# Kernel tuning notes

Measured on AMD Instinct MI355X. Metric: run time of the kernel, lower is better.

Reference implementation:

```python
import jax, jax.numpy as jnp
import numpy as np

BS, T, G, C = 64, 128, 36, 256
H = 256          # gaze LSTM hidden
P = 256          # spatial projected size
PT = 256         # temporal projected size
Q = 16           # queue size
NC = 10          # num classes
NEG = -1e9


def setup_inputs() -> dict:
    key = jax.random.key(0)
    ks = jax.random.split(key, 40)
    s = 0.02
    D = C + H
    inp = {
        'cnn_feat_seq': jax.random.normal(ks[0], (BS, T, G, C), jnp.float32),
        'gaze_seq': jax.random.normal(ks[1], (BS, T, 3), jnp.float32),
        # init-hidden / init-cell MLPs (Linear(3,H), Tanh, Linear(H,H), Tanh)
        'init_h_w1': jax.random.normal(ks[2], (H, 3)) * s, 'init_h_b1': jnp.zeros((H,)),
        'init_h_w2': jax.random.normal(ks[3], (H, H)) * s, 'init_h_b2': jnp.zeros((H,)),
        'init_c_w1': jax.random.normal(ks[4], (H, 3)) * s, 'init_c_b1': jnp.zeros((H,)),
        'init_c_w2': jax.random.normal(ks[5], (H, H)) * s, 'init_c_b2': jnp.zeros((H,)),
        # LSTM (input 3, hidden H), torch gate order i,f,g,o
        'lstm_wih': jax.random.normal(ks[6], (4 * H, 3)) * s, 'lstm_whh': jax.random.normal(ks[7], (4 * H, H)) * s,
        'lstm_bih': jnp.zeros((4 * H,)), 'lstm_bhh': jnp.zeros((4 * H,)),
        # spatial attention
        'sa_wl': jax.random.normal(ks[8], (P, H)) * s, 'sa_bl': jnp.zeros((P,)),
        'sa_wc': jax.random.normal(ks[9], (P, C)) * s, 'sa_bc': jnp.zeros((P,)),
        'sa_wz': jax.random.normal(ks[10], (P,)) * s,
        # temporal attention
        'ta_wl': jax.random.normal(ks[11], (PT, H)) * s, 'ta_bl': jnp.zeros((PT,)),
        'ta_wv': jax.random.normal(ks[12], (PT, C)) * s, 'ta_bv': jnp.zeros((PT,)),
        'ta_wz': jax.random.normal(ks[13], (PT,)) * s,
        # MLP classifier: Linear(D,D) -> Linear(D,D) -> Linear(D,NC), no nonlinearity
        'mlp_w1': jax.random.normal(ks[14], (D, D)) * s, 'mlp_b1': jnp.zeros((D,)),
        'mlp_w2': jax.random.normal(ks[15], (D, D)) * s, 'mlp_b2': jnp.zeros((D,)),
        'mlp_w3': jax.random.normal(ks[16], (NC, D)) * s, 'mlp_b3': jnp.zeros((NC,)),
    }
    return inp


def _forward(cnn_feat_seq, gaze_seq,
             init_h_w1, init_h_b1, init_h_w2, init_h_b2,
             init_c_w1, init_c_b1, init_c_w2, init_c_b2,
             lstm_wih, lstm_whh, lstm_bih, lstm_bhh,
             sa_wl, sa_bl, sa_wc, sa_bc, sa_wz,
             ta_wl, ta_bl, ta_wv, ta_bv, ta_wz,
             mlp_w1, mlp_b1, mlp_w2, mlp_b2, mlp_w3, mlp_b3):
    bs, num_frame = gaze_seq.shape[0], gaze_seq.shape[1]
    mean_gaze = jnp.mean(gaze_seq, axis=1)  # (bs, 3)
    # init MLP ends with Tanh, and forward applies F.tanh again
    h0 = jnp.tanh(jnp.tanh(jnp.tanh(mean_gaze @ init_h_w1.T + init_h_b1) @ init_h_w2.T + init_h_b2))
    c0 = jnp.tanh(jnp.tanh(jnp.tanh(mean_gaze @ init_c_w1.T + init_c_b1) @ init_c_w2.T + init_c_b2))
    buf_s0 = jnp.zeros((Q, bs, C), cnn_feat_seq.dtype)
    buf_h0 = jnp.zeros((Q, bs, H), cnn_feat_seq.dtype)
    qidx = jnp.arange(Q)

    def step(carry, xs):
        h, c, buf_s, buf_h, i = carry
        feat, gaze = xs  # (bs,G,C), (bs,3)
        # --- spatial additive attention over grids ---
        Hp = h @ sa_wl.T + sa_bl                                  # (bs,P)
        Vp = jnp.einsum('bgc,pc->bgp', feat, sa_wc) + sa_bc       # (bs,G,P)
        zs = jnp.tanh(Hp[:, None, :] + Vp) @ sa_wz                # (bs,G)
        sw = jax.nn.softmax(zs, axis=1)
        spat = jnp.einsum('bgc,bg->bc', feat, sw)                 # (bs,C)
        # --- rolling queues (newest last) ---
        buf_s = jnp.concatenate([buf_s[1:], spat[None]], axis=0)
        buf_h = jnp.concatenate([buf_h[1:], h[None]], axis=0)
        count = jnp.minimum(i + 1, Q)
        mask = qidx >= (Q - count)                                # (Q,) valid slots
        # --- temporal additive attention over queue ---
        Hq = jnp.einsum('qbh,ph->qbp', buf_h, ta_wl) + ta_bl
        Vq = jnp.einsum('qbc,pc->qbp', buf_s, ta_wv) + ta_bv
        zt = jnp.tanh(Hq + Vq) @ ta_wz                            # (Q,bs)
        zt = jnp.where(mask[:, None], zt, NEG)
        tw = jax.nn.softmax(zt, axis=0)
        temp = jnp.einsum('qbc,qb->bc', buf_s, tw)                # (bs,C)
        # --- one LSTM step on gaze ---
        gates = gaze @ lstm_wih.T + lstm_bih + h @ lstm_whh.T + lstm_bhh
        gi, gf, gg, go = jnp.split(gates, 4, axis=-1)
        c = jax.nn.sigmoid(gf) * c + jax.nn.sigmoid(gi) * jnp.tanh(gg)
        h = jax.nn.sigmoid(go) * jnp.tanh(c)
        # --- classifier on concat(temporal_feat, lstm_hidden) ---
        fc = jnp.concatenate([temp, h], axis=1)                   # (bs, C+H)
        pred = ((fc @ mlp_w1.T + mlp_b1) @ mlp_w2.T + mlp_b2) @ mlp_w3.T + mlp_b3
        return (h, c, buf_s, buf_h, i + 1), pred

    feats_t = jnp.swapaxes(cnn_feat_seq, 0, 1)  # (T,bs,G,C)
    gaze_t = jnp.swapaxes(gaze_seq, 0, 1)       # (T,bs,3)
    _, preds = jax.lax.scan(step, (h0, c0, buf_s0, buf_h0, jnp.int32(0)), (feats_t, gaze_t))
    # torch cats (1,bs,NC) pieces along dim=1 -> (1, T*bs, NC)
    return preds.reshape(1, num_frame * bs, NC)


def reference(cnn_feat_seq, gaze_seq,
              init_h_w1, init_h_b1, init_h_w2, init_h_b2,
              init_c_w1, init_c_b1, init_c_w2, init_c_b2,
              lstm_wih, lstm_whh, lstm_bih, lstm_bhh,
              sa_wl, sa_bl, sa_wc, sa_bc, sa_wz,
              ta_wl, ta_bl, ta_wv, ta_bv, ta_wz,
              mlp_w1, mlp_b1, mlp_w2, mlp_b2, mlp_w3, mlp_b3):
    return _forward(cnn_feat_seq, gaze_seq,
                    init_h_w1, init_h_b1, init_h_w2, init_h_b2,
                    init_c_w1, init_c_b1, init_c_w2, init_c_b2,
                    lstm_wih, lstm_whh, lstm_bih, lstm_bhh,
                    sa_wl, sa_bl, sa_wc, sa_bc, sa_wz,
                    ta_wl, ta_bl, ta_wv, ta_bv, ta_wz,
                    mlp_w1, mlp_b1, mlp_w2, mlp_b2, mlp_w3, mlp_b3)
```

## Files before the change

kernel.cpp:

```cpp
#include <hip/hip_runtime.h>
#include <cstdint>
#include <cstddef>

#define BSZ 64
#define TT  128
#define GG  36
#define CC  256
#define HH  256
#define QQ  16
#define NCLS 10
#define NROW 8192

using short8  = __attribute__((ext_vector_type(8))) short;
using f32x4   = __attribute__((ext_vector_type(4))) float;
using half2_t = __attribute__((ext_vector_type(2))) _Float16;
typedef unsigned int u32;
typedef unsigned short u16;

#define OFF_WI    0u
#define OFF_WF    131072u
#define OFF_WG    262144u
#define OFF_WO    393216u
#define OFF_SAWL  524288u
#define OFF_TAWL  655360u
#define OFF_TAWV  786432u
#define OFF_SAWC  917504u
#define OFF_W32   1048576u
#define OFF_WC    1069056u
#define OFF_BC    1089536u
#define OFF_H0F16 1089792u
#define OFF_C0    1122560u
#define OFF_HSEQ  1188096u
#define OFF_HSEQB 9642240u
#define OFF_HPSA  13869312u
#define OFF_HQ    22257920u
#define OFF_SPAT  30646528u
#define OFF_SPATB 39035136u
#define OFF_ZSC   43229440u
#define WS_NEEDED 43262208u

__device__ __forceinline__ float rcp_fast(float x){
#if __has_builtin(__builtin_amdgcn_rcpf)
  return __builtin_amdgcn_rcpf(x);
#else
  return 1.f/x;
#endif
}
__device__ __forceinline__ float fast_sig(float x){ return rcp_fast(1.f+__expf(-x)); }
__device__ __forceinline__ float fast_tanh(float x){ float e=__expf(2.f*x); return 1.f-2.f*rcp_fast(e+1.f); }
__device__ __forceinline__ u16 f2bf(float f){
  u32 u = __builtin_bit_cast(u32, f);
  u += 0x7fffu + ((u>>16)&1u);
  return (u16)(u>>16);
}
__device__ __forceinline__ float bf2f(u16 b){
  u32 u = ((u32)b)<<16; return __builtin_bit_cast(float, u);
}
__device__ __forceinline__ u32 cvtpk_bf16(float a, float b){
  u32 p;
  asm("v_cvt_pk_bf16_f32 %0, %1, %2" : "=v"(p) : "v"(a), "v"(b));
  return p;
}
__device__ __forceinline__ u32 packf16(float a, float b){
  half2_t h; h.x = (_Float16)a; h.y = (_Float16)b;
  return __builtin_bit_cast(u32, h);
}
__device__ __forceinline__ float dot2(u32 w, u32 h, float acc){
#if __has_builtin(__builtin_amdgcn_fdot2)
  return __builtin_amdgcn_fdot2(__builtin_bit_cast(half2_t, w),
                                __builtin_bit_cast(half2_t, h), acc, false);
#else
  half2_t a = __builtin_bit_cast(half2_t, w), b = __builtin_bit_cast(half2_t, h);
  return acc + (float)a.x*(float)b.x + (float)a.y*(float)b.y;
#endif
}
__device__ __forceinline__ f32x4 mfma16(short8 a, short8 b, f32x4 c){
  return __builtin_amdgcn_mfma_f32_16x16x32_bf16(a, b, c, 0, 0, 0);
}

__global__ void __launch_bounds__(256) k_prep1(const float* __restrict__ whh,
    const float* __restrict__ sawl, const float* __restrict__ tawl,
    const float* __restrict__ tawv, const float* __restrict__ sawc,
    const float* __restrict__ w3, const float* __restrict__ w2, char* ws){
  int blk = blockIdx.x, tid = threadIdx.x;
  if (blk < 512){
    u32* wq = (u32*)ws;
    for (int rr = 0; rr < 2; ++rr){
      int row = blk*2 + rr;
      float v  = whh[row*256 + tid];
      float vn = __shfl_down(v, 1);
      if ((tid & 1) == 0){
        int typ = row >> 8;
        int j   = row & 255;
        wq[typ*32768 + (tid>>1)*256 + j] = packf16(v, vn);
      }
    }
  } else if (blk < 544){
    int rel = blk - 512;
    int mat = rel >> 3;
    const float* src; u16* dst;
    if (mat==0){ src=sawl; dst=(u16*)(ws+OFF_SAWL); }
    else if (mat==1){ src=tawl; dst=(u16*)(ws+OFF_TAWL); }
    else if (mat==2){ src=tawv; dst=(u16*)(ws+OFF_TAWV); }
    else { src=sawc; dst=(u16*)(ws+OFF_SAWC); }
    int base = (rel & 7)*8192 + tid;
    for (int i = 0; i < 32; ++i){ int e = base + i*256; dst[e] = f2bf(src[e]); }
  } else {
    int idx = (blk-544)*256 + tid;
    int o = idx >> 9, k2 = idx & 511;
    float acc = 0.f;
    for (int m = 0; m < 512; ++m) acc = fmaf(w3[o*512+m], w2[m*512+k2], acc);
    ((float*)(ws+OFF_W32))[idx] = acc;
  }
}

__global__ void __launch_bounds__(256) k_prep2(const float* __restrict__ w1,
    const float* __restrict__ b1, const float* __restrict__ w3,
    const float* __restrict__ b2, const float* __restrict__ b3,
    const float* __restrict__ gaze,
    const float* __restrict__ ihw1, const float* __restrict__ ihb1,
    const float* __restrict__ ihw2, const float* __restrict__ ihb2,
    const float* __restrict__ icw1, const float* __restrict__ icb1,
    const float* __restrict__ icw2, const float* __restrict__ icb2,
    char* ws){
  int blk = blockIdx.x, tid = threadIdx.x;
  const float* W32 = (const float*)(ws+OFF_W32);
  if (blk < 20){
    int idx = blk*256 + tid; int o = idx>>9, k = idx&511;
    float acc = 0.f;
    for (int m = 0; m < 512; ++m) acc = fmaf(W32[o*512+m], w1[m*512+k], acc);
    ((float*)(ws+OFF_WC))[idx] = acc;
  } else if (blk == 20){
    if (tid < 10){
      float acc = b3[tid];
      for (int m = 0; m < 512; ++m) acc = fmaf(W32[tid*512+m], b1[m], acc);
      for (int m = 0; m < 512; ++m) acc = fmaf(w3[tid*512+m], b2[m], acc);
      ((float*)(ws+OFF_BC))[tid] = acc;
    }
  } else {
    int b = blk - 21;
    __shared__ float red0[128], red1[128], red2[128];
    __shared__ float mg[3];
    __shared__ float x1[256];
    if (tid < 128){
      const float* gp = gaze + b*384 + tid*3;
      red0[tid] = gp[0]; red1[tid] = gp[1]; red2[tid] = gp[2];
    }
    __syncthreads();
    for (int s = 64; s >= 1; s >>= 1){
      if (tid < s){ red0[tid]+=red0[tid+s]; red1[tid]+=red1[tid+s]; red2[tid]+=red2[tid+s]; }
      __syncthreads();
    }
    if (tid == 0){ mg[0]=red0[0]*(1.f/128.f); mg[1]=red1[0]*(1.f/128.f); mg[2]=red2[0]*(1.f/128.f); }
    __syncthreads();
    for (int which = 0; which < 2; ++which){
      const float* aw1 = which? icw1 : ihw1; const float* ab1 = which? icb1 : ihb1;
      const float* aw2 = which? icw2 : ihw2; const float* ab2 = which? icb2 : ihb2;
      float v = fast_tanh(fmaf(aw1[tid*3+2],mg[2], fmaf(aw1[tid*3+1],mg[1], fmaf(aw1[tid*3],mg[0], ab1[tid]))));
      x1[tid] = v;
      __syncthreads();
      float acc = ab2[tid];
      for (int k = 0; k < 256; ++k) acc = fmaf(aw2[tid*256+k], x1[k], acc);
      float h0 = fast_tanh(fast_tanh(acc));
      if (which == 0){
        float* hseq = (float*)(ws+OFF_HSEQ);
        hseq[(size_t)(0*64 + b)*256 + tid] = h0;
        float hn = __shfl_down(h0, 1);
        if ((tid&1)==0){
          ((u32*)(ws+OFF_HSEQB))[((size_t)(0*64+b)*256 + tid)>>1] = ((u32)f2bf(hn)<<16) | f2bf(h0);
          ((u32*)(ws+OFF_H0F16))[b*128 + (tid>>1)] = packf16(h0, hn);
        }
      } else {
        ((float*)(ws+OFF_C0))[b*256 + tid] = h0;
      }
      __syncthreads();
    }
  }
}

__global__ void __launch_bounds__(512, 2) k_lstm(const float* __restrict__ gaze,
    const float* __restrict__ wih, const float* __restrict__ bih,
    const float* __restrict__ bhh, char* ws){
  int b = blockIdx.x, tid = threadIdx.x;
  int half = tid >> 8;
  int j = tid & 255;
  __shared__ u32 lds_w[16*2048];
  __shared__ __align__(16) u32 hbuf[2][128];
  __shared__ float p_lds[256];
  __shared__ float g_lds[384];

  const u32* wq = (const u32*)ws;
  const u32* wA = wq + (half ? 1 : 0) * 32768;
  const u32* wB = wq + (half ? 3 : 2) * 32768;
  u32 w0[128], w1r[64];
#pragma unroll
  for (int c = 0; c < 128; ++c) w0[c] = wA[c*256 + j];
#pragma unroll
  for (int c = 0; c < 64; ++c)  w1r[c] = wB[c*256 + j];
#pragma unroll
  for (int cq = 0; cq < 16; ++cq)
#pragma unroll
    for (int q = 0; q < 4; ++q)
      lds_w[cq*2048 + tid*4 + q] = wB[(64 + cq*4 + q)*256 + j];

  if (tid < 384) g_lds[tid] = gaze[b*384 + tid];
  if (tid < 128) hbuf[0][tid] = ((const u32*)(ws+OFF_H0F16))[b*128 + tid];
  float creg = half ? ((const float*)(ws+OFF_C0))[b*256 + j] : 0.f;

  int rA = half ? 256 + j : j;
  int rB = half ? 768 + j : 512 + j;
  float baseA = bih[rA] + bhh[rA];
  float baseB = bih[rB] + bhh[rB];
  float uA0 = wih[rA*3], uA1 = wih[rA*3+1], uA2 = wih[rA*3+2];
  float uB0 = wih[rB*3], uB1 = wih[rB*3+1], uB2 = wih[rB*3+2];

  float* hseq = (float*)(ws+OFF_HSEQ);
  u32* hseqb = (u32*)(ws+OFF_HSEQB);
  __syncthreads();

  for (int t = 0; t < 128; ++t){
    int cur = t & 1, nxt = cur ^ 1;
    float g0 = g_lds[t*3], g1 = g_lds[t*3+1], g2 = g_lds[t*3+2];
    float aA0 = fmaf(uA2,g2, fmaf(uA1,g1, fmaf(uA0,g0, baseA))), aA1 = 0.f;
    float aB0 = fmaf(uB2,g2, fmaf(uB1,g1, fmaf(uB0,g0, baseB))), aB1 = 0.f;
#pragma unroll
    for (int c4 = 0; c4 < 32; ++c4){
      uint4 h4 = *reinterpret_cast<const uint4*>(&hbuf[cur][c4*4]);
      u32 wb0, wb1, wb2, wb3;
      if (c4 < 16){
        wb0 = w1r[c4*4]; wb1 = w1r[c4*4+1]; wb2 = w1r[c4*4+2]; wb3 = w1r[c4*4+3];
      } else {
        uint4 wv = *reinterpret_cast<const uint4*>(&lds_w[(c4-16)*2048 + tid*4]);
        wb0 = wv.x; wb1 = wv.y; wb2 = wv.z; wb3 = wv.w;
      }
      aA0 = dot2(w0[c4*4+0], h4.x, aA0); aB0 = dot2(wb0, h4.x, aB0);
      aA1 = dot2(w0[c4*4+1], h4.y, aA1); aB1 = dot2(wb1, h4.y, aB1);
      aA0 = dot2(w0[c4*4+2], h4.z, aA0); aB0 = dot2(wb2, h4.z, aB0);
      aA1 = dot2(w0[c4*4+3], h4.w, aA1); aB1 = dot2(wb3, h4.w, aB1);
    }
    float aA = aA0 + aA1, aB = aB0 + aB1;
    if (half == 0){
      p_lds[j] = fast_sig(aA) * fast_tanh(aB);
    }
    __syncthreads();
    if (half == 1){
      float p = p_lds[j];
      creg = fmaf(fast_sig(aA), creg, p);
      float hv = fast_sig(aB) * fast_tanh(creg);
      float hn = __shfl_down(hv, 1);
      if ((j & 1) == 0){
        hbuf[nxt][j>>1] = packf16(hv, hn);
        hseqb[(((size_t)(t+1)*64 + b)*256 + j)>>1] = ((u32)f2bf(hn)<<16) | f2bf(hv);
      }
      hseq[((size_t)(t+1)*64 + b)*256 + j] = hv;
    }
    __syncthreads();
  }
}

__global__ void __launch_bounds__(256) k_proj1(const float* __restrict__ sabl,
    const float* __restrict__ sabc, const float* __restrict__ tabl,
    const float* __restrict__ tabv, char* ws){
  int bx = blockIdx.x, which = blockIdx.y;
  const u16* A = (const u16*)(ws+OFF_HSEQB);
  const u16* B = (const u16*)(ws + (which? OFF_TAWL : OFF_SAWL));
  float* Out   = (float*)(ws + (which? OFF_HQ : OFF_HPSA));
  const float* bp1 = which? tabl : sabl;
  const float* bp2 = which? tabv : sabc;
  int tid = threadIdx.x, w = tid>>6, l = tid&63;
  int lr = l&15, lk = l>>4;
  int rb = bx*64;
  short8 afr[4][8];
#pragma unroll
  for (int m = 0; m < 4; ++m)
#pragma unroll
    for (int k = 0; k < 8; ++k)
      afr[m][k] = *(const short8*)(const void*)(A + (size_t)(rb + m*16 + lr)*256 + k*32 + lk*8);
#pragma unroll
  for (int n = 0; n < 4; ++n){
    int cb = w*64 + n*16;
    int col = cb + lr;
    float bias = bp1[col] + bp2[col];
    f32x4 a0 = {0.f,0.f,0.f,0.f}, a1 = a0, a2 = a0, a3 = a0;
#pragma unroll
    for (int k = 0; k < 8; ++k){
      short8 bf = *(const short8*)(const void*)(B + (size_t)col*256 + k*32 + lk*8);
      a0 = mfma16(afr[0][k], bf, a0);
      a1 = mfma16(afr[1][k], bf, a1);
      a2 = mfma16(afr[2][k], bf, a2);
      a3 = mfma16(afr[3][k], bf, a3);
    }
#pragma unroll
    for (int q = 0; q < 4; ++q){
      Out[(size_t)(rb + 0*16 + lk*4 + q)*256 + col] = a0[q] + bias;
      Out[(size_t)(rb + 1*16 + lk*4 + q)*256 + col] = a1[q] + bias;
      Out[(size_t)(rb + 2*16 + lk*4 + q)*256 + col] = a2[q] + bias;
      Out[(size_t)(rb + 3*16 + lk*4 + q)*256 + col] = a3[q] + bias;
    }
  }
}

__global__ void __launch_bounds__(256) k_spatial(const float* __restrict__ feat,
    const float* __restrict__ sawz, char* ws){
  int blk = blockIdx.x;
  int tid = threadIdx.x, w = tid>>6, l = tid&63;
  int lr = l&15, lk = l>>4;
  __shared__ __align__(16) u16 featb[84*264];
  __shared__ float hp[2][256];
  __shared__ float wzs[256];
  __shared__ float zsbuf[2][4][48];
  __shared__ float swl[2][36];
  const float* hpsa = (const float*)(ws+OFF_HPSA);
#pragma unroll
  for (int rr = 0; rr < 2; ++rr){
    int r = blk*2 + rr;
    int t = r >> 6, b = r & 63;
    const float* fb = feat + ((size_t)(b*128 + t))*9216;
#pragma unroll
    for (int i = 0; i < 9; ++i){
      int e = tid + i*256;
      int g = e >> 6, cp4 = e & 63;
      float4 v = *(const float4*)(fb + g*256 + cp4*4);
      uint2 pp;
      pp.x = cvtpk_bf16(v.x, v.y);
      pp.y = cvtpk_bf16(v.z, v.w);
      *reinterpret_cast<uint2*>(&featb[(rr*36 + g)*264 + cp4*4]) = pp;
    }
    hp[rr][tid] = hpsa[(size_t)r*256 + tid];
  }
  wzs[tid] = sawz[tid];
  __syncthreads();
  const u16* Bw = (const u16*)(ws+OFF_SAWC);
#pragma unroll
  for (int rr = 0; rr < 2; ++rr){
    short8 afr[3][8];
#pragma unroll
    for (int m = 0; m < 3; ++m)
#pragma unroll
      for (int k = 0; k < 8; ++k)
        afr[m][k] = *(const short8*)(const void*)(featb + (rr*36 + m*16 + lr)*264 + k*32 + lk*8);
    float zacc[3][4] = {{0.f}};
#pragma unroll
    for (int n = 0; n < 4; ++n){
      int col = w*64 + n*16 + lr;
      float hpl = hp[rr][col], wzv = wzs[col];
      f32x4 a0 = {0.f,0.f,0.f,0.f}, a1 = a0, a2 = a0;
#pragma unroll
      for (int k = 0; k < 8; ++k){
        short8 bf = *(const short8*)(const void*)(Bw + (size_t)col*256 + k*32 + lk*8);
        a0 = mfma16(afr[0][k], bf, a0);
        a1 = mfma16(afr[1][k], bf, a1);
        a2 = mfma16(afr[2][k], bf, a2);
      }
#pragma unroll
      for (int q = 0; q < 4; ++q){
        zacc[0][q] += fast_tanh(a0[q] + hpl)*wzv;
        zacc[1][q] += fast_tanh(a1[q] + hpl)*wzv;
        zacc[2][q] += fast_tanh(a2[q] + hpl)*wzv;
      }
    }
#pragma unroll
    for (int m = 0; m < 3; ++m)
#pragma unroll
      for (int q = 0; q < 4; ++q){
        float v = zacc[m][q];
        v += __shfl_xor(v, 1); v += __shfl_xor(v, 2);
        v += __shfl_xor(v, 4); v += __shfl_xor(v, 8);
        if (lr == 0) zsbuf[rr][w][m*16 + lk*4 + q] = v;
      }
  }
  __syncthreads();
  {
    int rr = w & 1;
    float z = (l < 36)? zsbuf[rr][0][l]+zsbuf[rr][1][l]+zsbuf[rr][2][l]+zsbuf[rr][3][l] : -1e30f;
    float mx = z;
    for (int d = 1; d < 64; d <<= 1) mx = fmaxf(mx, __shfl_xor(mx, d));
    float e = (l < 36)? __expf(z - mx) : 0.f;
    float s = e;
    for (int d = 1; d < 64; d <<= 1) s += __shfl_xor(s, d);
    if (w < 2 && l < 36) swl[rr][l] = e * rcp_fast(s);
  }
  __syncthreads();
#pragma unroll
  for (int rr = 0; rr < 2; ++rr){
    int r = blk*2 + rr;
    float acc = 0.f;
#pragma unroll
    for (int g = 0; g < 36; ++g)
      acc = fmaf(swl[rr][g], bf2f(featb[(rr*36 + g)*264 + tid]), acc);
    ((float*)(ws+OFF_SPAT))[(size_t)r*256 + tid] = acc;
    float an = __shfl_down(acc, 1);
    if ((tid&1)==0)
      ((u32*)(ws+OFF_SPATB))[((size_t)r*256 + tid)>>1] = cvtpk_bf16(acc, an);
  }
}

__global__ void __launch_bounds__(256) k_proj2(const float* __restrict__ tawz, char* ws){
  int bx = blockIdx.x;
  int tid = threadIdx.x, w = tid>>6, l = tid&63;
  int lr = l&15, lk = l>>4;
  int rb = bx*64;
  const u16* A = (const u16*)(ws+OFF_SPATB);
  const u16* B = (const u16*)(ws+OFF_TAWV);
  const float* Hq = (const float*)(ws+OFF_HQ);
  __shared__ float zbuf[4][64];
  short8 afr[4][8];
#pragma unroll
  for (int m = 0; m < 4; ++m)
#pragma unroll
    for (int k = 0; k < 8; ++k)
      afr[m][k] = *(const short8*)(const void*)(A + (size_t)(rb + m*16 + lr)*256 + k*32 + lk*8);
  float racc[4][4] = {{0.f}};
#pragma unroll
  for (int n = 0; n < 4; ++n){
    int col = w*64 + n*16 + lr;
    float tzl = tawz[col];
    f32x4 a0 = {0.f,0.f,0.f,0.f}, a1 = a0, a2 = a0, a3 = a0;
#pragma unroll
    for (int k = 0; k < 8; ++k){
      short8 bf = *(const short8*)(const void*)(B + (size_t)col*256 + k*32 + lk*8);
      a0 = mfma16(afr[0][k], bf, a0);
      a1 = mfma16(afr[1][k], bf, a1);
      a2 = mfma16(afr[2][k], bf, a2);
      a3 = mfma16(afr[3][k], bf, a3);
    }
#pragma unroll
    for (int q = 0; q < 4; ++q){
      racc[0][q] += fast_tanh(a0[q] + Hq[(size_t)(rb + 0*16 + lk*4 + q)*256 + col]) * tzl;
      racc[1][q] += fast_tanh(a1[q] + Hq[(size_t)(rb + 1*16 + lk*4 + q)*256 + col]) * tzl;
      racc[2][q] += fast_tanh(a2[q] + Hq[(size_t)(rb + 2*16 + lk*4 + q)*256 + col]) * tzl;
      racc[3][q] += fast_tanh(a3[q] + Hq[(size_t)(rb + 3*16 + lk*4 + q)*256 + col]) * tzl;
    }
  }
#pragma unroll
  for (int m = 0; m < 4; ++m)
#pragma unroll
    for (int q = 0; q < 4; ++q){
      float v = racc[m][q];
      v += __shfl_xor(v, 1); v += __shfl_xor(v, 2);
      v += __shfl_xor(v, 4); v += __shfl_xor(v, 8);
      if (lr == 0) zbuf[w][m*16 + lk*4 + q] = v;
    }
  __syncthreads();
  if (tid < 64)
    ((float*)(ws+OFF_ZSC))[rb + tid] = zbuf[0][tid]+zbuf[1][tid]+zbuf[2][tid]+zbuf[3][tid];
}

__global__ void __launch_bounds__(256) k_final(float* __restrict__ out, char* ws){
  int bx = blockIdx.x;
  int b = bx & 63, tb = bx >> 6;
  int t0 = tb*8;
  int tid = threadIdx.x;
  int wv = tid>>6, l = tid&63;
  __shared__ float spw[23][256];
  __shared__ float zw[23];
  __shared__ float WcL[5120];
  __shared__ float bcL[10];
  __shared__ float w16[16];
  __shared__ float wpart[4][10];
  const float* spat = (const float*)(ws+OFF_SPAT);
  const float* zsc  = (const float*)(ws+OFF_ZSC);
  const float* hseq = (const float*)(ws+OFF_HSEQ);
  const float* Wc   = (const float*)(ws+OFF_WC);
#pragma unroll
  for (int i = 0; i < 20; ++i) WcL[tid + i*256] = Wc[tid + i*256];
  if (tid < 10) bcL[tid] = ((const float*)(ws+OFF_BC))[tid];
  for (int i = 0; i < 23; ++i){
    int tau = t0 - 15 + i;
    spw[i][tid] = (tau >= 0)? spat[(size_t)(tau*64 + b)*256 + tid] : 0.f;
  }
  if (tid < 23){
    int tau = t0 - 15 + tid;
    zw[tid] = (tau >= 0)? zsc[tau*64 + b] : -1e9f;
  }
  __syncthreads();
  for (int dt = 0; dt < 8; ++dt){
    int t = t0 + dt;
    if (wv == 0 && l < 16){
      float z = zw[dt + l];
      float mx = z;
      mx = fmaxf(mx, __shfl_xor(mx,1)); mx = fmaxf(mx, __shfl_xor(mx,2));
      mx = fmaxf(mx, __shfl_xor(mx,4)); mx = fmaxf(mx, __shfl_xor(mx,8));
      float e = __expf(z - mx);
      float s = e;
      s += __shfl_xor(s,1); s += __shfl_xor(s,2); s += __shfl_xor(s,4); s += __shfl_xor(s,8);
      w16[l] = e / s;
    }
    __syncthreads();
    float temp = 0.f;
#pragma unroll
    for (int qi = 0; qi < 16; ++qi) temp = fmaf(w16[qi], spw[dt+qi][tid], temp);
    float hc = hseq[(size_t)((t+1)*64 + b)*256 + tid];
    float po[10];
#pragma unroll
    for (int o = 0; o < 10; ++o){
      float v = fmaf(temp, WcL[o*512 + tid], hc*WcL[o*512 + 256 + tid]);
      v += __shfl_xor(v,1);  v += __shfl_xor(v,2);  v += __shfl_xor(v,4);
      v += __shfl_xor(v,8);  v += __shfl_xor(v,16); v += __shfl_xor(v,32);
      po[o] = v;
    }
    if (l == 0){
#pragma unroll
      for (int o = 0; o < 10; ++o) wpart[wv][o] = po[o];
    }
    __syncthreads();
    if (tid < 10)
      out[(size_t)(t*64 + b)*10 + tid] = wpart[0][tid]+wpart[1][tid]+wpart[2][tid]+wpart[3][tid] + bcL[tid];
    __syncthreads();
  }
}

extern "C" void kernel_launch(void* const* d_in, const int* in_sizes, int n_in,
                              void* d_out, int out_size, void* d_ws, size_t ws_size,
                              hipStream_t stream){
  const float* feat = (const float*)d_in[0];
  const float* gaze = (const float*)d_in[1];
  const float* ihw1 = (const float*)d_in[2];  const float* ihb1 = (const float*)d_in[3];
  const float* ihw2 = (const float*)d_in[4];  const float* ihb2 = (const float*)d_in[5];
  const float* icw1 = (const float*)d_in[6];  const float* icb1 = (const float*)d_in[7];
  const float* icw2 = (const float*)d_in[8];  const float* icb2 = (const float*)d_in[9];
  const float* wih  = (const float*)d_in[10]; const float* whh  = (const float*)d_in[11];
  const float* bih  = (const float*)d_in[12]; const float* bhh  = (const float*)d_in[13];
  const float* sawl = (const float*)d_in[14]; const float* sabl = (const float*)d_in[15];
  const float* sawc = (const float*)d_in[16]; const float* sabc = (const float*)d_in[17];
  const float* sawz = (const float*)d_in[18];
  const float* tawl = (const float*)d_in[19]; const float* tabl = (const float*)d_in[20];
  const float* tawv = (const float*)d_in[21]; const float* tabv = (const float*)d_in[22];
  const float* tawz = (const float*)d_in[23];
  const float* w1 = (const float*)d_in[24]; const float* b1 = (const float*)d_in[25];
  const float* w2 = (const float*)d_in[26]; const float* b2 = (const float*)d_in[27];
  const float* w3 = (const float*)d_in[28]; const float* b3 = (const float*)d_in[29];
  char* ws = (char*)d_ws;
  float* out = (float*)d_out;
  if (ws_size < (size_t)WS_NEEDED) return;

  k_prep1<<<dim3(564), dim3(256), 0, stream>>>(whh, sawl, tawl, tawv, sawc, w3, w2, ws);
  k_prep2<<<dim3(85), dim3(256), 0, stream>>>(w1, b1, w3, b2, b3, gaze,
      ihw1, ihb1, ihw2, ihb2, icw1, icb1, icw2, icb2, ws);
  k_lstm<<<dim3(64), dim3(512), 0, stream>>>(gaze, wih, bih, bhh, ws);
  k_proj1<<<dim3(128, 2), dim3(256), 0, stream>>>(sabl, sabc, tabl, tabv, ws);
  k_spatial<<<dim3(4096), dim3(256), 0, stream>>>(feat, sawz, ws);
  k_proj2<<<dim3(128), dim3(256), 0, stream>>>(tawz, ws);
  k_final<<<dim3(1024), dim3(256), 0, stream>>>(out, ws);
}
```

Baseline: 527.0 us.

## Make spatial attention kernel persistent with LDS-resident weights and prefetch

The spatial attention kernel now runs 256 persistent blocks of 32 rows each instead of 4096 blocks of 2 rows. Each block loads the 128KB bf16 sa_wc weight matrix into LDS once, so the MFMA B operands no longer come from global/L2 on every row. The next row's features are prefetched into registers while the current row computes. LDS layouts are XOR-swizzled to avoid bank conflicts, and the weight prep writes the matching swizzled layout. The cost is one block per CU with heavy LDS use, which limits latency hiding, and the loop is serialised by several barriers per row.

```diff
diff --git a/kernel.cpp b/kernel.cpp
--- a/kernel.cpp
+++ b/kernel.cpp
@@ -10,6 +10,7 @@
 #define QQ  16
 #define NCLS 10
 #define NROW 8192
+#define SP_ROWS 32
 
 using short8  = __attribute__((ext_vector_type(8))) short;
 using f32x4   = __attribute__((ext_vector_type(4))) float;
@@ -104,7 +105,15 @@
     else if (mat==2){ src=tawv; dst=(u16*)(ws+OFF_TAWV); }
     else { src=sawc; dst=(u16*)(ws+OFF_SAWC); }
     int base = (rel & 7)*8192 + tid;
-    for (int i = 0; i < 32; ++i){ int e = base + i*256; dst[e] = f2bf(src[e]); }
+    if (mat < 3){
+      for (int i = 0; i < 32; ++i){ int e = base + i*256; dst[e] = f2bf(src[e]); }
+    } else {
+      for (int i = 0; i < 32; ++i){
+        int e = base + i*256;
+        int col = e >> 8, kk = e & 255;
+        dst[col*256 + (kk ^ ((col&7)<<3))] = f2bf(src[e]);
+      }
+    }
   } else {
     int idx = (blk-544)*256 + tid;
     int o = idx >> 9, k2 = idx & 511;
@@ -300,54 +309,81 @@
   }
 }
 
-__global__ void __launch_bounds__(256) k_spatial(const float* __restrict__ feat,
+__global__ void __launch_bounds__(256, 1) k_spatial(const float* __restrict__ feat,
     const float* __restrict__ sawz, char* ws){
-  int blk = blockIdx.x;
-  int tid = threadIdx.x, w = tid>>6, l = tid&63;
+  __shared__ __align__(16) u16 Blds[256*256];
+  __shared__ __align__(16) u16 featb[48*256];
+  __shared__ __align__(16) float hp[256];
+  __shared__ float wzs[256];
+  __shared__ float zsbuf[4][48];
+  __shared__ float swl[36];
+  int bx = blockIdx.x, tid = threadIdx.x, w = tid>>6, l = tid&63;
   int lr = l&15, lk = l>>4;
-  __shared__ __align__(16) u16 featb[84*264];
-  __shared__ float hp[2][256];
-  __shared__ float wzs[256];
-  __shared__ float zsbuf[2][4][48];
-  __shared__ float swl[2][36];
   const float* hpsa = (const float*)(ws+OFF_HPSA);
-#pragma unroll
-  for (int rr = 0; rr < 2; ++rr){
-    int r = blk*2 + rr;
-    int t = r >> 6, b = r & 63;
-    const float* fb = feat + ((size_t)(b*128 + t))*9216;
-#pragma unroll
-    for (int i = 0; i < 9; ++i){
-      int e = tid + i*256;
-      int g = e >> 6, cp4 = e & 63;
-      float4 v = *(const float4*)(fb + g*256 + cp4*4);
+
+  {
+    const uint4* gB = (const uint4*)(ws + OFF_SAWC);
+    uint4* lB = (uint4*)Blds;
+#pragma unroll
+    for (int it = 0; it < 32; ++it)
+      lB[it*256 + tid] = gB[it*256 + tid];
+  }
+  {
+    u32* fz = (u32*)featb;
+#pragma unroll
+    for (int z = 0; z < 6; ++z) fz[36*128 + z*256 + tid] = 0;
+  }
+  wzs[tid] = sawz[tid];
+
+  float4 pf[9]; float4 ph;
+  {
+    int r0 = bx*SP_ROWS;
+    int t = r0>>6, b = r0&63;
+    const float4* fb = (const float4*)(feat + ((size_t)(b*128 + t))*9216);
+#pragma unroll
+    for (int ii = 0; ii < 9; ++ii) pf[ii] = fb[tid + ii*256];
+    ph = (tid < 64)? ((const float4*)(hpsa + (size_t)r0*256))[tid] : make_float4(0.f,0.f,0.f,0.f);
+  }
+  __syncthreads();
+
+  for (int i = 0; i < SP_ROWS; ++i){
+    int r = bx*SP_ROWS + i;
+#pragma unroll
+    for (int ii = 0; ii < 9; ++ii){
+      int e = tid + ii*256;
+      int g = e >> 6, c4 = e & 63;
       uint2 pp;
-      pp.x = cvtpk_bf16(v.x, v.y);
-      pp.y = cvtpk_bf16(v.z, v.w);
-      *reinterpret_cast<uint2*>(&featb[(rr*36 + g)*264 + cp4*4]) = pp;
-    }
-    hp[rr][tid] = hpsa[(size_t)r*256 + tid];
-  }
-  wzs[tid] = sawz[tid];
-  __syncthreads();
-  const u16* Bw = (const u16*)(ws+OFF_SAWC);
-#pragma unroll
-  for (int rr = 0; rr < 2; ++rr){
+      pp.x = cvtpk_bf16(pf[ii].x, pf[ii].y);
+      pp.y = cvtpk_bf16(pf[ii].z, pf[ii].w);
+      *reinterpret_cast<uint2*>((u32*)featb + g*128 + ((c4*2) ^ ((g&7)<<2))) = pp;
+    }
+    if (tid < 64) *reinterpret_cast<float4*>(hp + tid*4) = ph;
+    __syncthreads();
+    if (i + 1 < SP_ROWS){
+      int rn = r + 1;
+      int t = rn>>6, b = rn&63;
+      const float4* fb = (const float4*)(feat + ((size_t)(b*128 + t))*9216);
+#pragma unroll
+      for (int ii = 0; ii < 9; ++ii) pf[ii] = fb[tid + ii*256];
+      if (tid < 64) ph = ((const float4*)(hpsa + (size_t)rn*256))[tid];
+    }
     short8 afr[3][8];
 #pragma unroll
     for (int m = 0; m < 3; ++m)
 #pragma unroll
-      for (int k = 0; k < 8; ++k)
-        afr[m][k] = *(const short8*)(const void*)(featb + (rr*36 + m*16 + lr)*264 + k*32 + lk*8);
+      for (int k = 0; k < 8; ++k){
+        int g = m*16 + lr;
+        afr[m][k] = *(const short8*)(const void*)(featb + g*256 + ((k*32 + lk*8) ^ ((g&7)<<3)));
+      }
     float zacc[3][4] = {{0.f}};
 #pragma unroll
     for (int n = 0; n < 4; ++n){
       int col = w*64 + n*16 + lr;
-      float hpl = hp[rr][col], wzv = wzs[col];
+      float hpl = hp[col], wzv = wzs[col];
       f32x4 a0 = {0.f,0.f,0.f,0.f}, a1 = a0, a2 = a0;
 #pragma unroll
       for (int k = 0; k < 8; ++k){
-        short8 bf = *(const short8*)(const void*)(Bw + (size_t)col*256 + k*32 + lk*8);
+        short8 bf = *(const short8*)(const void*)(Blds + col*256 + ((k*32 + lk*8) ^ ((col&7)<<3)));
         a0 = mfma16(afr[0][k], bf, a0);
         a1 = mfma16(afr[1][k], bf, a1);
         a2 = mfma16(afr[2][k], bf, a2);
@@ -366,32 +402,30 @@
         float v = zacc[m][q];
         v += __shfl_xor(v, 1); v += __shfl_xor(v, 2);
         v += __shfl_xor(v, 4); v += __shfl_xor(v, 8);
-        if (lr == 0) zsbuf[rr][w][m*16 + lk*4 + q] = v;
-      }
-  }
-  __syncthreads();
-  {
-    int rr = w & 1;
-    float z = (l < 36)? zsbuf[rr][0][l]+zsbuf[rr][1][l]+zsbuf[rr][2][l]+zsbuf[rr][3][l] : -1e30f;
-    float mx = z;
-    for (int d = 1; d < 64; d <<= 1) mx = fmaxf(mx, __shfl_xor(mx, d));
-    float e = (l < 36)? __expf(z - mx) : 0.f;
-    float s = e;
-    for (int d = 1; d < 64; d <<= 1) s += __shfl_xor(s, d);
-    if (w < 2 && l < 36) swl[rr][l] = e * rcp_fast(s);
-  }
-  __syncthreads();
-#pragma unroll
-  for (int rr = 0; rr < 2; ++rr){
-    int r = blk*2 + rr;
-    float acc = 0.f;
-#pragma unroll
-    for (int g = 0; g < 36; ++g)
-      acc = fmaf(swl[rr][g], bf2f(featb[(rr*36 + g)*264 + tid]), acc);
-    ((float*)(ws+OFF_SPAT))[(size_t)r*256 + tid] = acc;
-    float an = __shfl_down(acc, 1);
-    if ((tid&1)==0)
-      ((u32*)(ws+OFF_SPATB))[((size_t)r*256 + tid)>>1] = cvtpk_bf16(acc, an);
+        if (lr == 0) zsbuf[w][m*16 + lk*4 + q] = v;
+      }
+    __syncthreads();
+    if (w == 0){
+      float z = (l < 36)? zsbuf[0][l]+zsbuf[1][l]+zsbuf[2][l]+zsbuf[3][l] : -1e30f;
+      float mx = z;
+      for (int d = 1; d < 64; d <<= 1) mx = fmaxf(mx, __shfl_xor(mx, d));
+      float e = (l < 36)? __expf(z - mx) : 0.f;
+      float s = e;
+      for (int d = 1; d < 64; d <<= 1) s += __shfl_xor(s, d);
+      if (l < 36) swl[l] = e * rcp_fast(s);
+    }
+    __syncthreads();
+    {
+      float acc = 0.f;
+#pragma unroll
+      for (int g = 0; g < 36; ++g)
+        acc = fmaf(swl[g], bf2f(featb[g*256 + (tid ^ ((g&7)<<3))]), acc);
+      ((float*)(ws+OFF_SPAT))[(size_t)r*256 + tid] = acc;
+      float an = __shfl_down(acc, 1);
+      if ((tid & 1) == 0)
+        ((u32*)(ws+OFF_SPATB))[((size_t)r*256 + tid)>>1] = cvtpk_bf16(acc, an);
+    }
+    __syncthreads();
   }
 }
 
@@ -539,7 +573,7 @@
       ihw1, ihb1, ihw2, ihb2, icw1, icb1, icw2, icb2, ws);
   k_lstm<<<dim3(64), dim3(512), 0, stream>>>(gaze, wih, bih, bhh, ws);
   k_proj1<<<dim3(128, 2), dim3(256), 0, stream>>>(sabl, sabc, tabl, tabv, ws);
-  k_spatial<<<dim3(4096), dim3(256), 0, stream>>>(feat, sawz, ws);
+  k_spatial<<<dim3(256), dim3(256), 0, stream>>>(feat, sawz, ws);
   k_proj2<<<dim3(128), dim3(256), 0, stream>>>(tawz, ws);
   k_final<<<dim3(1024), dim3(256), 0, stream>>>(out, ws);
 }
```

Measured after the change: 517.5 us. Within noise of the previous version (-1.8%).
